# Performance work log

Measured on AMD Instinct MI355X. Metric: run time of the kernel, lower is better.

The kernel has to match this reference:

```python
import jax, jax.numpy as jnp
import numpy as np

HEADS = 8
DIM_HEAD = 64


def setup_inputs() -> dict:
    key = jax.random.key(0)
    ks = jax.random.split(key, 6)
    dim = 512
    inner = HEADS * DIM_HEAD  # 512
    x = jax.random.normal(ks[0], (4, 4096, dim), dtype=jnp.float32)
    s = 1.0 / np.sqrt(dim)
    Wq = jax.random.normal(ks[1], (dim, inner), dtype=jnp.float32) * s
    Wk = jax.random.normal(ks[2], (dim, inner), dtype=jnp.float32) * s
    Wv = jax.random.normal(ks[3], (dim, inner), dtype=jnp.float32) * s
    Wo = jax.random.normal(ks[4], (inner, dim), dtype=jnp.float32) * (1.0 / np.sqrt(inner))
    bo = jax.random.normal(ks[5], (dim,), dtype=jnp.float32) * 0.01
    return {"x": x, "Wq": Wq, "Wk": Wk, "Wv": Wv, "Wo": Wo, "bo": bo}


def reference(x, Wq, Wk, Wv, Wo, bo):
    b, n, _ = x.shape
    h, d = HEADS, DIM_HEAD
    # project and split heads: [b, h, n, d]
    q = (x @ Wq).reshape(b, n, h, d).transpose(0, 2, 1, 3)
    k = (x @ Wk).reshape(b, n, h, d).transpose(0, 2, 1, 3)
    v = (x @ Wv).reshape(b, n, h, d).transpose(0, 2, 1, 3)
    q = jax.nn.softmax(q, axis=-1)
    k = jax.nn.softmax(k, axis=-1)
    context = jnp.einsum('bhnd,bhne->bhde', k, v)  # small d x d per head
    out = jnp.einsum('bhnd,bhde->bhne', q, context)
    out = out.transpose(0, 2, 1, 3).reshape(b, n, h * d)
    return out @ Wo + bo
```

## Files before the change

### kernel.cpp

```cpp
#include <hip/hip_runtime.h>

typedef unsigned short u16;
typedef unsigned int   u32;
typedef __bf16 bf16x8 __attribute__((ext_vector_type(8)));
typedef float  f32x4  __attribute__((ext_vector_type(4)));
typedef u16    u16x8  __attribute__((ext_vector_type(8)));
typedef u16    u16x4  __attribute__((ext_vector_type(4)));

__device__ __forceinline__ float b2f(u16 h) {
  return __builtin_bit_cast(float, ((u32)h) << 16);
}
__device__ __forceinline__ u16 f2b(float f) {
  u32 u = __builtin_bit_cast(u32, f);
  u32 r = u + 0x7FFFu + ((u >> 16) & 1u);
  return (u16)(r >> 16);
}

#define GLD_AS1(p) ((const __attribute__((address_space(1))) void*)(p))
#define LDS_AS3(p) ((__attribute__((address_space(3))) void*)(p))

__global__ void gemm_qkv_kernel(const u16* __restrict__ A, const u16* __restrict__ Bt,
                                u16* __restrict__ qb, float* __restrict__ ctxp) {
  const int K = 512;
  __shared__ u16 smem[16384];
  const int id = blockIdx.x;
  const int tn = id >> 7;
  const int tm = (id & 7) * 16 + ((id >> 3) & 15);
  const int tileM = tm * 128;
  const int t = threadIdx.x;
  const int lane = t & 63;
  const int wave = t >> 6;
  const int mbase = (wave >> 1) * 64;
  const int nbase = (wave & 1) * 64;
  const int fm = lane & 15;
  const int kg = lane >> 4;
  const bool is_q = (tn < 4);
  const int j = tn - 4;

  f32x4 acc[4][4];
#pragma unroll
  for (int i = 0; i < 4; ++i)
#pragma unroll
    for (int jj = 0; jj < 4; ++jj) acc[i][jj] = (f32x4){0.f, 0.f, 0.f, 0.f};

  auto stage = [&](int buf, int k0) {
    u16* As = smem + buf * 8192;
    u16* Bs = As + 4096;
#pragma unroll
    for (int p = 0; p < 2; ++p) {
      int c = p * 256 + t;
      int r = c >> 2;
      int g = (c & 3) ^ ((r >> 1) & 3);
      const u16* ga = A + (size_t)(tileM + r) * K + (k0 + g * 8);
      __builtin_amdgcn_global_load_lds(GLD_AS1(ga), LDS_AS3(As + c * 8), 16, 0, 0);
      int brow = is_q ? (tn * 128 + r) : (512 + j * 64 + r + (r >> 6) * 448);
      const u16* gb = Bt + (size_t)brow * K + (k0 + g * 8);
      __builtin_amdgcn_global_load_lds(GLD_AS1(gb), LDS_AS3(Bs + c * 8), 16, 0, 0);
    }
  };

  stage(0, 0);
  __syncthreads();

  for (int kk = 0; kk < 16; ++kk) {
    const int cur = kk & 1;
    if (kk < 15) stage(cur ^ 1, (kk + 1) * 32);

    const u16* As = smem + cur * 8192;
    const u16* Bs = As + 4096;
    bf16x8 af[4], bfr[4];
#pragma unroll
    for (int mi = 0; mi < 4; ++mi) {
      int m = mbase + mi * 16 + fm;
      int sg = kg ^ ((m >> 1) & 3);
      af[mi] = *(const bf16x8*)(As + m * 32 + sg * 8);
    }
#pragma unroll
    for (int ni = 0; ni < 4; ++ni) {
      int n = nbase + ni * 16 + fm;
      int sg = kg ^ ((n >> 1) & 3);
      bfr[ni] = *(const bf16x8*)(Bs + n * 32 + sg * 8);
    }
#pragma unroll
    for (int mi = 0; mi < 4; ++mi)
#pragma unroll
      for (int ni = 0; ni < 4; ++ni)
        acc[mi][ni] = __builtin_amdgcn_mfma_f32_16x16x32_bf16(af[mi], bfr[ni],
                                                              acc[mi][ni], 0, 0, 0);
    __syncthreads();
  }

  const int rq = lane >> 4;

  float inv[4][4];
  const bool do_sm = is_q || ((wave & 1) == 0);
  if (do_sm) {
#pragma unroll
    for (int mi = 0; mi < 4; ++mi)
#pragma unroll
      for (int ni = 0; ni < 4; ++ni)
#pragma unroll
        for (int reg = 0; reg < 4; ++reg)
          acc[mi][ni][reg] = __expf(acc[mi][ni][reg]);
#pragma unroll
    for (int mi = 0; mi < 4; ++mi)
#pragma unroll
      for (int reg = 0; reg < 4; ++reg) {
        float s = acc[mi][0][reg] + acc[mi][1][reg] + acc[mi][2][reg] + acc[mi][3][reg];
        s += __shfl_xor(s, 1);
        s += __shfl_xor(s, 2);
        s += __shfl_xor(s, 4);
        s += __shfl_xor(s, 8);
        inv[mi][reg] = 1.f / s;
      }
  } else {
#pragma unroll
    for (int mi = 0; mi < 4; ++mi)
#pragma unroll
      for (int reg = 0; reg < 4; ++reg) inv[mi][reg] = 1.f;
  }

  if (is_q) {
#pragma unroll
    for (int mi = 0; mi < 4; ++mi)
#pragma unroll
      for (int ni = 0; ni < 4; ++ni)
#pragma unroll
        for (int reg = 0; reg < 4; ++reg) {
          int gr = tileM + mbase + mi * 16 + rq * 4 + reg;
          int gc = tn * 128 + nbase + ni * 16 + fm;
          qb[(size_t)gr * 512 + gc] = f2b(acc[mi][ni][reg] * inv[mi][reg]);
        }
    return;
  }

  u16* T = smem;
  f32x4 cacc[4];
#pragma unroll
  for (int i = 0; i < 4; ++i) cacc[i] = (f32x4){0.f, 0.f, 0.f, 0.f};

#pragma unroll
  for (int ph = 0; ph < 2; ++ph) {
    if ((wave >> 1) == ph) {
#pragma unroll
      for (int mi = 0; mi < 4; ++mi)
#pragma unroll
        for (int ni = 0; ni < 4; ++ni) {
          u16x4 o;
#pragma unroll
          for (int reg = 0; reg < 4; ++reg)
            o[reg] = f2b(acc[mi][ni][reg] * inv[mi][reg]);
          int c = nbase + ni * 16 + fm;
          *(u16x4*)(T + c * 72 + mi * 16 + rq * 4) = o;
        }
    }
    __syncthreads();
#pragma unroll
    for (int kk = 0; kk < 2; ++kk) {
      bf16x8 afc = *(const bf16x8*)(T + (wave * 16 + fm) * 72 + kk * 32 + kg * 8);
#pragma unroll
      for (int et = 0; et < 4; ++et) {
        bf16x8 bfc = *(const bf16x8*)(T + (64 + et * 16 + fm) * 72 + kk * 32 + kg * 8);
        cacc[et] = __builtin_amdgcn_mfma_f32_16x16x32_bf16(afc, bfc, cacc[et], 0, 0, 0);
      }
    }
    __syncthreads();
  }

  const int b = tm >> 5;
  const int s = tm & 31;
  float* cp = ctxp + ((size_t)s * 32 + b * 8 + j) * 4096;
#pragma unroll
  for (int et = 0; et < 4; ++et)
#pragma unroll
    for (int reg = 0; reg < 4; ++reg)
      cp[(wave * 16 + rq * 4 + reg) * 64 + et * 16 + fm] = cacc[et][reg];
}

__global__ void prep_all_kernel(const float* __restrict__ x, const float* __restrict__ Wq,
                                const float* __restrict__ Wk, const float* __restrict__ Wv,
                                const float* __restrict__ Wo, u16* __restrict__ xb,
                                u16* __restrict__ Wt, u16* __restrict__ Wot) {
  __shared__ u16 tr[64 * 72];
  const int id = blockIdx.x;
  const int t = threadIdx.x;

  if (id < 4096) {
    int i = (id * 256 + t) * 8;
    float4 a = *(const float4*)(x + i);
    float4 b = *(const float4*)(x + i + 4);
    u16x8 o;
    o[0] = f2b(a.x); o[1] = f2b(a.y); o[2] = f2b(a.z); o[3] = f2b(a.w);
    o[4] = f2b(b.x); o[5] = f2b(b.y); o[6] = f2b(b.z); o[7] = f2b(b.w);
    *(u16x8*)(xb + i) = o;
    return;
  }
  const float* W;
  u16* dst;
  int n0, k0;
  if (id < 4288) {
    int tile = id - 4096;
    n0 = (tile >> 3) * 64;
    k0 = (tile & 7) * 64;
    W = (n0 < 512) ? Wq : ((n0 < 1024) ? Wk : Wv);
    dst = Wt;
  } else {
    int tile = id - 4288;
    n0 = (tile >> 3) * 64;
    k0 = (tile & 7) * 64;
    W = Wo;
    dst = Wot;
  }
  int cin = (n0 & 511);
  int c = t & 63;
  int r0 = t >> 6;
#pragma unroll
  for (int i = 0; i < 16; ++i) {
    int r = r0 * 16 + i;
    tr[c * 72 + r] = f2b(W[(size_t)(k0 + r) * 512 + cin + c]);
  }
  __syncthreads();
#pragma unroll
  for (int jj = 0; jj < 2; ++jj) {
    int idx = jj * 256 + t;
    int row = idx >> 3;
    int seg = idx & 7;
    u16x8 val = *(const u16x8*)(tr + row * 72 + seg * 8);
    *(u16x8*)(dst + (size_t)(n0 + row) * 512 + k0 + seg * 8) = val;
  }
}

__global__ void ctx_reduce_kernel(const float* __restrict__ ctxp, u16* __restrict__ ctxb) {
  const int id = blockIdx.x;
  const int bh = id >> 2;
  const int chunk = id & 3;
  const int t = threadIdx.x;
  const int idx = chunk * 1024 + t * 4;
  f32x4 s = (f32x4){0.f, 0.f, 0.f, 0.f};
#pragma unroll
  for (int p = 0; p < 32; ++p)
    s += *(const f32x4*)(ctxp + ((size_t)p * 32 + bh) * 4096 + idx);
  u16x4 o;
#pragma unroll
  for (int jj = 0; jj < 4; ++jj) o[jj] = f2b(s[jj]);
  *(u16x4*)(ctxb + (size_t)bh * 4096 + idx) = o;
}

__global__ void ctxm_kernel(const u16* __restrict__ ctxb, const u16* __restrict__ Wot,
                            u16* __restrict__ Mt) {
  __shared__ u16 ctxd[64 * 72];
  const int id = blockIdx.x;
  const int bh = id >> 2;
  const int cq = id & 3;
  const int b = bh >> 3, h = bh & 7;
  const int t = threadIdx.x;
  const int lane = t & 63;
  const int wave = t >> 6;
  const int fm = lane & 15;
  const int kg = lane >> 4;
  const int rq = lane >> 4;

  {
    int base = t * 16;
    int d = base >> 6, e = base & 63;
    u16x8 v0 = *(const u16x8*)(ctxb + (size_t)bh * 4096 + base);
    u16x8 v1 = *(const u16x8*)(ctxb + (size_t)bh * 4096 + base + 8);
    *(u16x8*)(ctxd + d * 72 + e) = v0;
    *(u16x8*)(ctxd + d * 72 + e + 8) = v1;
  }
  __syncthreads();

  f32x4 acc[2][4];
#pragma unroll
  for (int i = 0; i < 2; ++i)
#pragma unroll
    for (int jj = 0; jj < 4; ++jj) acc[i][jj] = (f32x4){0.f, 0.f, 0.f, 0.f};

#pragma unroll
  for (int ks = 0; ks < 2; ++ks) {
    bf16x8 bfr[4];
#pragma unroll
    for (int dt = 0; dt < 4; ++dt)
      bfr[dt] = *(const bf16x8*)(ctxd + (dt * 16 + fm) * 72 + ks * 32 + kg * 8);
#pragma unroll
    for (int mi = 0; mi < 2; ++mi) {
      int c = cq * 128 + wave * 32 + mi * 16 + fm;
      bf16x8 af = *(const bf16x8*)(Wot + (size_t)c * 512 + h * 64 + ks * 32 + kg * 8);
#pragma unroll
      for (int dt = 0; dt < 4; ++dt)
        acc[mi][dt] = __builtin_amdgcn_mfma_f32_16x16x32_bf16(af, bfr[dt],
                                                              acc[mi][dt], 0, 0, 0);
    }
  }

  u16* mb = Mt + (size_t)b * 512 * 512;
#pragma unroll
  for (int mi = 0; mi < 2; ++mi)
#pragma unroll
    for (int dt = 0; dt < 4; ++dt)
#pragma unroll
      for (int reg = 0; reg < 4; ++reg) {
        int c = cq * 128 + wave * 32 + mi * 16 + rq * 4 + reg;
        mb[(size_t)c * 512 + h * 64 + dt * 16 + fm] = f2b(acc[mi][dt][reg]);
      }
}

__global__ void gemm_out_kernel(const u16* __restrict__ A, const u16* __restrict__ Mt,
                                float* __restrict__ Cout, const float* __restrict__ bias) {
  const int K = 512, N = 512;
  __shared__ u16 smem[12288];
  const int id = blockIdx.x;
  const int tn = id >> 8;
  const int tm = (id & 7) * 32 + ((id >> 3) & 31);
  const int tileN = tn * 128;
  const int tileM = tm * 64;
  const u16* Bt = Mt + (size_t)(tm >> 6) * 512 * 512;
  const int t = threadIdx.x;
  const int lane = t & 63;
  const int wave = t >> 6;
  const int mbase = (wave >> 1) * 32;
  const int nbase = (wave & 1) * 64;
  const int fm = lane & 15;
  const int kg = lane >> 4;

  f32x4 acc[2][4];
#pragma unroll
  for (int i = 0; i < 2; ++i)
#pragma unroll
    for (int jj = 0; jj < 4; ++jj) acc[i][jj] = (f32x4){0.f, 0.f, 0.f, 0.f};

  auto stage = [&](int buf, int k0) {
    u16* As = smem + buf * 6144;
    u16* Bs = As + 2048;
    {
      int c = t;
      int r = c >> 2;
      int g = (c & 3) ^ ((r >> 1) & 3);
      const u16* ga = A + (size_t)(tileM + r) * K + (k0 + g * 8);
      __builtin_amdgcn_global_load_lds(GLD_AS1(ga), LDS_AS3(As + c * 8), 16, 0, 0);
    }
#pragma unroll
    for (int p = 0; p < 2; ++p) {
      int c = p * 256 + t;
      int r = c >> 2;
      int g = (c & 3) ^ ((r >> 1) & 3);
      const u16* gb = Bt + (size_t)(tileN + r) * K + (k0 + g * 8);
      __builtin_amdgcn_global_load_lds(GLD_AS1(gb), LDS_AS3(Bs + c * 8), 16, 0, 0);
    }
  };

  stage(0, 0);
  __syncthreads();

  for (int kk = 0; kk < 16; ++kk) {
    const int cur = kk & 1;
    if (kk < 15) stage(cur ^ 1, (kk + 1) * 32);

    const u16* As = smem + cur * 6144;
    const u16* Bs = As + 2048;
    bf16x8 af[2], bfr[4];
#pragma unroll
    for (int mi = 0; mi < 2; ++mi) {
      int m = mbase + mi * 16 + fm;
      int sg = kg ^ ((m >> 1) & 3);
      af[mi] = *(const bf16x8*)(As + m * 32 + sg * 8);
    }
#pragma unroll
    for (int ni = 0; ni < 4; ++ni) {
      int n = nbase + ni * 16 + fm;
      int sg = kg ^ ((n >> 1) & 3);
      bfr[ni] = *(const bf16x8*)(Bs + n * 32 + sg * 8);
    }
#pragma unroll
    for (int mi = 0; mi < 2; ++mi)
#pragma unroll
      for (int ni = 0; ni < 4; ++ni)
        acc[mi][ni] = __builtin_amdgcn_mfma_f32_16x16x32_bf16(af[mi], bfr[ni],
                                                              acc[mi][ni], 0, 0, 0);
    __syncthreads();
  }

  const int rq = lane >> 4;
#pragma unroll
  for (int mi = 0; mi < 2; ++mi)
#pragma unroll
    for (int ni = 0; ni < 4; ++ni)
#pragma unroll
      for (int reg = 0; reg < 4; ++reg) {
        int gr = tileM + mbase + mi * 16 + rq * 4 + reg;
        int gc = tileN + nbase + ni * 16 + fm;
        Cout[(size_t)gr * N + gc] = acc[mi][ni][reg] + bias[gc];
      }
}

extern "C" void kernel_launch(void* const* d_in, const int* in_sizes, int n_in,
                              void* d_out, int out_size, void* d_ws, size_t ws_size,
                              hipStream_t stream) {
  const float* x  = (const float*)d_in[0];
  const float* Wq = (const float*)d_in[1];
  const float* Wk = (const float*)d_in[2];
  const float* Wv = (const float*)d_in[3];
  const float* Wo = (const float*)d_in[4];
  const float* bo = (const float*)d_in[5];

  char* w = (char*)d_ws;
  u16* xb   = (u16*)w;    w += (size_t)16384 * 512 * 2;
  u16* Wt   = (u16*)w;    w += (size_t)1536 * 512 * 2;
  u16* Wot  = (u16*)w;    w += (size_t)512 * 512 * 2;
  u16* qbuf = (u16*)w;    w += (size_t)16384 * 512 * 2;
  float* ctxp = (float*)w; w += (size_t)32 * 32 * 4096 * 4;
  u16* ctxb = (u16*)w;    w += (size_t)32 * 4096 * 2;
  u16* Mt   = (u16*)w;    w += (size_t)4 * 512 * 512 * 2;

  prep_all_kernel<<<4352, 256, 0, stream>>>(x, Wq, Wk, Wv, Wo, xb, Wt, Wot);
  gemm_qkv_kernel<<<1536, 256, 0, stream>>>(xb, Wt, qbuf, ctxp);
  ctx_reduce_kernel<<<128, 256, 0, stream>>>(ctxp, ctxb);
  ctxm_kernel<<<128, 256, 0, stream>>>(ctxb, Wot, Mt);
  gemm_out_kernel<<<1024, 256, 0, stream>>>(qbuf, Mt, (float*)d_out, bo);
}
```

Measured before the change: 155.3 us.

## Triple-buffer LDS staging in QKV and output GEMMs with vmcnt-based waits

Both GEMM kernels move from a double-buffered to a triple-buffered LDS pipeline, prefetching two k-tiles ahead with direct global-to-LDS loads. Each iteration waits only on the older in-flight loads through explicit vmcnt counts, then uses a barrier after fragment reads before overwriting the consumed buffer. The aim is to hide global load latency behind MFMA work. In exchange it uses more LDS per block, which may lower occupancy, and correctness now depends on hand-counted vmcnt values.

```diff
diff --git a/kernel.cpp b/kernel.cpp
--- a/kernel.cpp
+++ b/kernel.cpp
@@ -22,7 +22,7 @@
 __global__ void gemm_qkv_kernel(const u16* __restrict__ A, const u16* __restrict__ Bt,
                                 u16* __restrict__ qb, float* __restrict__ ctxp) {
   const int K = 512;
-  __shared__ u16 smem[16384];
+  __shared__ u16 smem[24576];
   const int id = blockIdx.x;
   const int tn = id >> 7;
   const int tm = (id & 7) * 16 + ((id >> 3) & 15);
@@ -60,11 +60,15 @@
   };
 
   stage(0, 0);
-  __syncthreads();
-
+  stage(1, 32);
+  stage(2, 64);
+
+  int cur = 0;
   for (int kk = 0; kk < 16; ++kk) {
-    const int cur = kk & 1;
-    if (kk < 15) stage(cur ^ 1, (kk + 1) * 32);
+    if (kk <= 13)      asm volatile("s_waitcnt vmcnt(8)" ::: "memory");
+    else if (kk == 14) asm volatile("s_waitcnt vmcnt(4)" ::: "memory");
+    else               asm volatile("s_waitcnt vmcnt(0)" ::: "memory");
+    __builtin_amdgcn_s_barrier();
 
     const u16* As = smem + cur * 8192;
     const u16* Bs = As + 4096;
@@ -81,13 +85,19 @@
       int sg = kg ^ ((n >> 1) & 3);
       bfr[ni] = *(const bf16x8*)(Bs + n * 32 + sg * 8);
     }
+    asm volatile("s_waitcnt lgkmcnt(0)" ::: "memory");
+    __builtin_amdgcn_sched_barrier(0);
+    __builtin_amdgcn_s_barrier();
+
+    if (kk <= 12) stage(cur, (kk + 3) * 32);
+
 #pragma unroll
     for (int mi = 0; mi < 4; ++mi)
 #pragma unroll
       for (int ni = 0; ni < 4; ++ni)
         acc[mi][ni] = __builtin_amdgcn_mfma_f32_16x16x32_bf16(af[mi], bfr[ni],
                                                               acc[mi][ni], 0, 0, 0);
-    __syncthreads();
+    cur = (cur == 2) ? 0 : cur + 1;
   }
 
   const int rq = lane >> 4;
@@ -308,7 +318,7 @@
 __global__ void gemm_out_kernel(const u16* __restrict__ A, const u16* __restrict__ Mt,
                                 float* __restrict__ Cout, const float* __restrict__ bias) {
   const int K = 512, N = 512;
-  __shared__ u16 smem[12288];
+  __shared__ u16 smem[18432];
   const int id = blockIdx.x;
   const int tn = id >> 8;
   const int tm = (id & 7) * 32 + ((id >> 3) & 31);
@@ -350,11 +360,15 @@
   };
 
   stage(0, 0);
-  __syncthreads();
-
+  stage(1, 32);
+  stage(2, 64);
+
+  int cur = 0;
   for (int kk = 0; kk < 16; ++kk) {
-    const int cur = kk & 1;
-    if (kk < 15) stage(cur ^ 1, (kk + 1) * 32);
+    if (kk <= 13)      asm volatile("s_waitcnt vmcnt(6)" ::: "memory");
+    else if (kk == 14) asm volatile("s_waitcnt vmcnt(3)" ::: "memory");
+    else               asm volatile("s_waitcnt vmcnt(0)" ::: "memory");
+    __builtin_amdgcn_s_barrier();
 
     const u16* As = smem + cur * 6144;
     const u16* Bs = As + 2048;
@@ -371,13 +385,19 @@
       int sg = kg ^ ((n >> 1) & 3);
       bfr[ni] = *(const bf16x8*)(Bs + n * 32 + sg * 8);
     }
+    asm volatile("s_waitcnt lgkmcnt(0)" ::: "memory");
+    __builtin_amdgcn_sched_barrier(0);
+    __builtin_amdgcn_s_barrier();
+
+    if (kk <= 12) stage(cur, (kk + 3) * 32);
+
 #pragma unroll
     for (int mi = 0; mi < 2; ++mi)
 #pragma unroll
       for (int ni = 0; ni < 4; ++ni)
         acc[mi][ni] = __builtin_amdgcn_mfma_f32_16x16x32_bf16(af[mi], bfr[ni],
                                                               acc[mi][ni], 0, 0, 0);
-    __syncthreads();
+    cur = (cur == 2) ? 0 : cur + 1;
   }
 
   const int rq = lane >> 4;
```

Result: no change. 154.0 us (-0.8%).
